# Kernel optimization log

Measured on AMD Instinct MI355X. Metric: run time of the kernel, lower is better.

The kernel has to match this reference:

```python
import jax, jax.numpy as jnp
import numpy as np


def setup_inputs() -> dict:
    key = jax.random.key(0)
    N, H, CH, T = 4, 8, 64, 2048
    qkv = jax.random.normal(key, (N, 3 * H * CH, T), dtype=jnp.float32)
    return {"qkv": qkv, "n_heads": H}


def reference(qkv, n_heads):
    bs, width, length = qkv.shape
    ch = width // (3 * n_heads)
    q, k, v = jnp.split(qkv, 3, axis=1)  # each [bs, H*ch, T]
    q = q.reshape(bs * n_heads, ch, length)
    k = k.reshape(bs * n_heads, ch, length)
    v = v.reshape(bs * n_heads, ch, length)
    scale = 1.0 / jnp.sqrt(jnp.sqrt(jnp.asarray(ch, dtype=qkv.dtype)))
    # [bs*H, T, T] score matrix (non-flash, materialized as in the original)
    weight = jnp.einsum('bct,bcs->bts', q * scale, k * scale)
    weight = jax.nn.softmax(weight.astype(jnp.float32), axis=-1).astype(qkv.dtype)
    a = jnp.einsum('bts,bcs->bct', weight, v)  # [bs*H, ch, T]
    return a.reshape(bs, n_heads * ch, length)
```

## Files before the change

### kernel.cpp

```cpp
#include <hip/hip_runtime.h>


typedef __bf16 bf8v __attribute__((ext_vector_type(8)));
typedef float f16v __attribute__((ext_vector_type(16)));
typedef int i4 __attribute__((ext_vector_type(4)));

#define SEQ 2048
#define DD 64
#define NHEADS 32
#define QBLK 128
#define SBLK 64
#define NTILES (SEQ / SBLK)
#define TILEK (SBLK * DD)
#define NTHR 256

#define KSC 0.35355339059327373f
#define QSC (0.35355339059327373f * 1.4426950408889634f)

#if __has_builtin(__builtin_amdgcn_exp2f)
#define EXP2(x) __builtin_amdgcn_exp2f(x)
#else
#define EXP2(x) exp2f(x)
#endif

__device__ __forceinline__ void gload16(i4& dst, const __bf16* p) {
    asm volatile("global_load_dwordx4 %0, %1, off" : "=&v"(dst) : "v"(p));
}

#define VMWAIT0() do { asm volatile("s_waitcnt vmcnt(0)" ::: "memory"); \
                       __builtin_amdgcn_sched_barrier(0); } while (0)
#define SBAR() __builtin_amdgcn_sched_barrier(0)

#if __has_builtin(__builtin_amdgcn_permlane32_swap)
typedef int i2v __attribute__((ext_vector_type(2)));
__device__ __forceinline__ void plswap(unsigned& a, unsigned& b) {
    i2v r = __builtin_amdgcn_permlane32_swap((int)a, (int)b, false, false);
    a = (unsigned)r.x;
    b = (unsigned)r.y;
}
#else
__device__ __forceinline__ void plswap(unsigned& a, unsigned& b) {
    asm volatile("v_permlane32_swap_b32 %0, %1" : "+v"(a), "+v"(b));
}
#endif

__global__ void prep_kernel(const float* __restrict__ qkv,
                            __bf16* __restrict__ KT, __bf16* __restrict__ Vb) {
    const int bx = blockIdx.x, tid = threadIdx.x;
    if (bx < 256) {
        const int head = bx >> 3, sblk = bx & 7;
        const int b = head >> 3, h = head & 7;
        const float* kp = qkv + (size_t)(b * 1536 + 512 + h * 64) * SEQ;
        __bf16* dst = KT + (size_t)head * SEQ * DD;
        const int s = sblk * 256 + tid;
#pragma unroll
        for (int c0 = 0; c0 < DD; c0 += 8) {
            bf8v v;
#pragma unroll
            for (int j = 0; j < 8; ++j)
                v[j] = (__bf16)(kp[(size_t)(c0 + j) * SEQ + s] * KSC);
            *(bf8v*)(dst + (size_t)s * DD + c0) = v;
        }
    } else {
        const int job = bx - 256;
        const int head = job >> 4, part = job & 15;
        const int b = head >> 3, h = head & 7;
        const float* vp = qkv + (size_t)(b * 1536 + 1024 + h * 64) * SEQ;
        __bf16* dst = Vb + (size_t)head * DD * SEQ;
#pragma unroll
        for (int i = 0; i < 4; ++i) {
            const int e = part * 8192 + (i * 256 + tid) * 8;
            const float4* f = (const float4*)(vp + e);
            float4 a = f[0], c = f[1];
            bf8v o;
            o[0] = (__bf16)a.x; o[1] = (__bf16)a.y; o[2] = (__bf16)a.z; o[3] = (__bf16)a.w;
            o[4] = (__bf16)c.x; o[5] = (__bf16)c.y; o[6] = (__bf16)c.z; o[7] = (__bf16)c.w;
            *(bf8v*)(dst + e) = o;
        }
    }
}

__device__ __forceinline__ bf8v ldswz(const __bf16* base, int r, int c16) {
    return *(const bf8v*)(base + r * DD + (((c16) ^ (r & 7)) << 3));
}

__global__ __launch_bounds__(NTHR, 2) void attn_kernel(
    const float* __restrict__ qkv, const __bf16* __restrict__ KT,
    const __bf16* __restrict__ Vb, float* __restrict__ out)
{
    __shared__ __bf16 KL[2][TILEK];
    __shared__ __bf16 VL[2][TILEK];

    const int tid = threadIdx.x;
    const int wid = tid >> 6;
    const int lane = tid & 63;
    const int hi = lane >> 5;
    const int l31 = lane & 31;

    const int bid = blockIdx.x;
    const int bx = (bid & 7) * 64 + (bid >> 3);
    const int head = bx >> 4;
    const int t0 = (bx & 15) * QBLK;
    const int b = head >> 3, h = head & 7;

    const float* qp = qkv + (size_t)(b * 1536 + h * 64) * SEQ;
    const __bf16* kt = KT + (size_t)head * SEQ * DD;
    const __bf16* vb = Vb + (size_t)head * DD * SEQ;
    float* op = out + (size_t)head * DD * SEQ;

    const int sp  = tid & 7;
    const int sr  = tid >> 3;
    const int scs = sp ^ (sr & 7);
    const __bf16* kg0 = kt + sr * DD + (scs << 3);
    const __bf16* kg1 = kt + (sr + 32) * DD + (scs << 3);
    const __bf16* vg0 = vb + (size_t)sr * SEQ + (scs << 3);
    const __bf16* vg1 = vb + (size_t)(sr + 32) * SEQ + (scs << 3);
    const int l0 = sr * DD + (sp << 3);
    const int l1 = (sr + 32) * DD + (sp << 3);

    i4 rk0, rk1, rv0, rv1;

    SBAR();
    gload16(rk0, kg0);
    gload16(rk1, kg1);
    gload16(rv0, vg0);
    gload16(rv1, vg1);
    SBAR();

    const int tq = t0 + wid * 32 + l31;
    bf8v qf[4];
#pragma unroll
    for (int kb = 0; kb < 4; ++kb) {
        bf8v q;
#pragma unroll
        for (int j = 0; j < 8; ++j)
            q[j] = (__bf16)(qp[(size_t)(kb * 16 + hi * 8 + j) * SEQ + tq] * QSC);
        qf[kb] = q;
    }

    f16v Oacc[2];
    Oacc[0] = (f16v)0.0f;
    Oacc[1] = (f16v)0.0f;
    float lp[4] = {0.f, 0.f, 0.f, 0.f};

    VMWAIT0();
    *(i4*)&KL[0][l0] = rk0;  *(i4*)&KL[0][l1] = rk1;
    *(i4*)&VL[0][l0] = rv0;  *(i4*)&VL[0][l1] = rv1;
    __syncthreads();

    for (int it = 0; it < NTILES; ++it) {
        const int cb = it & 1;
        const __bf16* kcu = KL[cb];
        const __bf16* vcu = VL[cb];
        const bool more = (it + 1 < NTILES);

        if (more) {
            const int nx = it + 1;
            SBAR();
            gload16(rk0, kg0 + nx * TILEK);
            gload16(rk1, kg1 + nx * TILEK);
            gload16(rv0, vg0 + nx * SBLK);
            gload16(rv1, vg1 + nx * SBLK);
            SBAR();
        }

        bf8v ka[2][4];
#pragma unroll
        for (int sb = 0; sb < 2; ++sb)
#pragma unroll
            for (int kb = 0; kb < 4; ++kb)
                ka[sb][kb] = ldswz(kcu, sb * 32 + l31, 2 * kb + hi);

        f16v S[2];
        S[0] = (f16v)0.0f;
        S[1] = (f16v)0.0f;
        __builtin_amdgcn_s_setprio(1);
#pragma unroll
        for (int kb = 0; kb < 4; ++kb) {
            S[0] = __builtin_amdgcn_mfma_f32_32x32x16_bf16(ka[0][kb], qf[kb], S[0], 0, 0, 0);
            S[1] = __builtin_amdgcn_mfma_f32_32x32x16_bf16(ka[1][kb], qf[kb], S[1], 0, 0, 0);
        }
        __builtin_amdgcn_s_setprio(0);

        bf8v vf[2][4];
#pragma unroll
        for (int vcb = 0; vcb < 2; ++vcb)
#pragma unroll
            for (int kb = 0; kb < 4; ++kb)
                vf[vcb][kb] = ldswz(vcu, vcb * 32 + l31, 2 * kb + hi);

        unsigned pd[2][4][2];
#pragma unroll
        for (int sb = 0; sb < 2; ++sb)
#pragma unroll
            for (int q = 0; q < 4; ++q) {
                float e0 = EXP2(S[sb][4 * q + 0]);
                float e1 = EXP2(S[sb][4 * q + 1]);
                float e2 = EXP2(S[sb][4 * q + 2]);
                float e3 = EXP2(S[sb][4 * q + 3]);
                lp[q] += (e0 + e1) + (e2 + e3);
                union { __bf16 h[2]; unsigned u; } p0, p1;
                p0.h[0] = (__bf16)e0; p0.h[1] = (__bf16)e1;
                p1.h[0] = (__bf16)e2; p1.h[1] = (__bf16)e3;
                pd[sb][q][0] = p0.u;
                pd[sb][q][1] = p1.u;
            }

#pragma unroll
        for (int sb = 0; sb < 2; ++sb)
#pragma unroll
            for (int m = 0; m < 2; ++m) {
                plswap(pd[sb][2 * m][0], pd[sb][2 * m + 1][0]);
                plswap(pd[sb][2 * m][1], pd[sb][2 * m + 1][1]);
            }

        if (more) {
            VMWAIT0();
            __bf16* kn = (__bf16*)KL[cb ^ 1];
            __bf16* vn = (__bf16*)VL[cb ^ 1];
            *(i4*)&kn[l0] = rk0;  *(i4*)&kn[l1] = rk1;
            *(i4*)&vn[l0] = rv0;  *(i4*)&vn[l1] = rv1;
            __syncthreads();
        }

        asm volatile("s_nop 2" :::);

        __builtin_amdgcn_s_setprio(1);
#pragma unroll
        for (int sb = 0; sb < 2; ++sb)
#pragma unroll
            for (int m = 0; m < 2; ++m) {
                const int kb = 2 * sb + m;
                union { unsigned u[4]; bf8v b; } f;
                f.u[0] = pd[sb][2 * m][0];
                f.u[1] = pd[sb][2 * m][1];
                f.u[2] = pd[sb][2 * m + 1][0];
                f.u[3] = pd[sb][2 * m + 1][1];
                Oacc[0] = __builtin_amdgcn_mfma_f32_32x32x16_bf16(vf[0][kb], f.b, Oacc[0], 0, 0, 0);
                Oacc[1] = __builtin_amdgcn_mfma_f32_32x32x16_bf16(vf[1][kb], f.b, Oacc[1], 0, 0, 0);
            }
        __builtin_amdgcn_s_setprio(0);
    }

    float l = (lp[0] + lp[1]) + (lp[2] + lp[3]);
    l += __shfl_xor(l, 32);
    const float rl = 1.0f / l;
#pragma unroll
    for (int cbk = 0; cbk < 2; ++cbk)
#pragma unroll
        for (int r = 0; r < 16; ++r) {
            const int row = cbk * 32 + (r & 3) + 8 * (r >> 2) + 4 * hi;
            op[(size_t)row * SEQ + tq] = Oacc[cbk][r] * rl;
        }
}

extern "C" void kernel_launch(void* const* d_in, const int* in_sizes, int n_in,
                              void* d_out, int out_size, void* d_ws, size_t ws_size,
                              hipStream_t stream) {
    const float* qkv = (const float*)d_in[0];
    float* out = (float*)d_out;
    __bf16* KT = (__bf16*)d_ws;
    __bf16* Vb = KT + (size_t)NHEADS * SEQ * DD;
    prep_kernel<<<dim3(256 + 512), dim3(NTHR), 0, stream>>>(qkv, KT, Vb);
    attn_kernel<<<dim3(NHEADS * (SEQ / QBLK)), dim3(NTHR), 0, stream>>>(qkv, KT, Vb, out);
}
```

Measured before the change: 64.76 us.

## Split key sequence across two wave groups per block and combine via LDS

Doubles the block to 512 threads and has two groups of four waves each process alternating key/value tiles for the same 128 queries. Partial outputs and row sums are merged through shared memory at the end. K/V fragment loads from LDS are moved inline next to their MFMAs to cut register pressure and allow higher occupancy. This raises the wave count per query block and the LDS use to 64KB, at the cost of an extra reduction step and more LDS traffic.

```diff
diff --git a/kernel.cpp b/kernel.cpp
--- a/kernel.cpp
+++ b/kernel.cpp
@@ -10,9 +10,9 @@
 #define NHEADS 32
 #define QBLK 128
 #define SBLK 64
-#define NTILES (SEQ / SBLK)
+#define NTILES 32
 #define TILEK (SBLK * DD)
-#define NTHR 256
+#define NTHR 512
 
 #define KSC 0.35355339059327373f
 #define QSC (0.35355339059327373f * 1.4426950408889634f)
@@ -84,15 +84,20 @@
     return *(const bf8v*)(base + r * DD + (((c16) ^ (r & 7)) << 3));
 }
 
-__global__ __launch_bounds__(NTHR, 2) void attn_kernel(
+__global__ __launch_bounds__(NTHR, 4) void attn_kernel(
     const float* __restrict__ qkv, const __bf16* __restrict__ KT,
     const __bf16* __restrict__ Vb, float* __restrict__ out)
 {
-    __shared__ __bf16 KL[2][TILEK];
-    __shared__ __bf16 VL[2][TILEK];
+    __shared__ __align__(16) char pool[65536];
+    __bf16* KLg = (__bf16*)pool;
+    __bf16* VLg = (__bf16*)(pool + 32768);
+    float* comb  = (float*)pool;
+    float* combl = (float*)(pool + 33280);
 
     const int tid = threadIdx.x;
     const int wid = tid >> 6;
+    const int gg  = wid >> 2;
+    const int qw  = wid & 3;
     const int lane = tid & 63;
     const int hi = lane >> 5;
     const int l31 = lane & 31;
@@ -108,8 +113,9 @@
     const __bf16* vb = Vb + (size_t)head * DD * SEQ;
     float* op = out + (size_t)head * DD * SEQ;
 
-    const int sp  = tid & 7;
-    const int sr  = tid >> 3;
+    const int g256 = tid & 255;
+    const int sp  = g256 & 7;
+    const int sr  = g256 >> 3;
     const int scs = sp ^ (sr & 7);
     const __bf16* kg0 = kt + sr * DD + (scs << 3);
     const __bf16* kg1 = kt + (sr + 32) * DD + (scs << 3);
@@ -121,13 +127,13 @@
     i4 rk0, rk1, rv0, rv1;
 
     SBAR();
-    gload16(rk0, kg0);
-    gload16(rk1, kg1);
-    gload16(rv0, vg0);
-    gload16(rv1, vg1);
+    gload16(rk0, kg0 + gg * TILEK);
+    gload16(rk1, kg1 + gg * TILEK);
+    gload16(rv0, vg0 + gg * SBLK);
+    gload16(rv1, vg1 + gg * SBLK);
     SBAR();
 
-    const int tq = t0 + wid * 32 + l31;
+    const int tq = t0 + qw * 32 + l31;
     bf8v qf[4];
 #pragma unroll
     for (int kb = 0; kb < 4; ++kb) {
@@ -144,60 +150,47 @@
     float lp[4] = {0.f, 0.f, 0.f, 0.f};
 
     VMWAIT0();
-    *(i4*)&KL[0][l0] = rk0;  *(i4*)&KL[0][l1] = rk1;
-    *(i4*)&VL[0][l0] = rv0;  *(i4*)&VL[0][l1] = rv1;
+    {
+        __bf16* k0 = KLg + (2 * gg) * TILEK;
+        __bf16* v0 = VLg + (2 * gg) * TILEK;
+        *(i4*)&k0[l0] = rk0;  *(i4*)&k0[l1] = rk1;
+        *(i4*)&v0[l0] = rv0;  *(i4*)&v0[l1] = rv1;
+    }
     __syncthreads();
 
-    for (int it = 0; it < NTILES; ++it) {
+    for (int it = 0; it < NTILES / 2; ++it) {
         const int cb = it & 1;
-        const __bf16* kcu = KL[cb];
-        const __bf16* vcu = VL[cb];
-        const bool more = (it + 1 < NTILES);
+        const __bf16* kcu = KLg + (2 * gg + cb) * TILEK;
+        const __bf16* vcu = VLg + (2 * gg + cb) * TILEK;
+        const bool more = (it + 1 < NTILES / 2);
 
         if (more) {
-            const int nx = it + 1;
+            const int tg = 2 * (it + 1) + gg;
             SBAR();
-            gload16(rk0, kg0 + nx * TILEK);
-            gload16(rk1, kg1 + nx * TILEK);
-            gload16(rv0, vg0 + nx * SBLK);
-            gload16(rv1, vg1 + nx * SBLK);
+            gload16(rk0, kg0 + tg * TILEK);
+            gload16(rk1, kg1 + tg * TILEK);
+            gload16(rv0, vg0 + tg * SBLK);
+            gload16(rv1, vg1 + tg * SBLK);
             SBAR();
         }
 
-        bf8v ka[2][4];
-#pragma unroll
-        for (int sb = 0; sb < 2; ++sb)
-#pragma unroll
-            for (int kb = 0; kb < 4; ++kb)
-                ka[sb][kb] = ldswz(kcu, sb * 32 + l31, 2 * kb + hi);
-
-        f16v S[2];
-        S[0] = (f16v)0.0f;
-        S[1] = (f16v)0.0f;
-        __builtin_amdgcn_s_setprio(1);
-#pragma unroll
-        for (int kb = 0; kb < 4; ++kb) {
-            S[0] = __builtin_amdgcn_mfma_f32_32x32x16_bf16(ka[0][kb], qf[kb], S[0], 0, 0, 0);
-            S[1] = __builtin_amdgcn_mfma_f32_32x32x16_bf16(ka[1][kb], qf[kb], S[1], 0, 0, 0);
-        }
-        __builtin_amdgcn_s_setprio(0);
-
-        bf8v vf[2][4];
-#pragma unroll
-        for (int vcb = 0; vcb < 2; ++vcb)
-#pragma unroll
-            for (int kb = 0; kb < 4; ++kb)
-                vf[vcb][kb] = ldswz(vcu, vcb * 32 + l31, 2 * kb + hi);
-
         unsigned pd[2][4][2];
 #pragma unroll
-        for (int sb = 0; sb < 2; ++sb)
+        for (int sb = 0; sb < 2; ++sb) {
+            f16v S = (f16v)0.0f;
+            __builtin_amdgcn_s_setprio(1);
+#pragma unroll
+            for (int kb = 0; kb < 4; ++kb) {
+                bf8v a = ldswz(kcu, sb * 32 + l31, 2 * kb + hi);
+                S = __builtin_amdgcn_mfma_f32_32x32x16_bf16(a, qf[kb], S, 0, 0, 0);
+            }
+            __builtin_amdgcn_s_setprio(0);
 #pragma unroll
             for (int q = 0; q < 4; ++q) {
-                float e0 = EXP2(S[sb][4 * q + 0]);
-                float e1 = EXP2(S[sb][4 * q + 1]);
-                float e2 = EXP2(S[sb][4 * q + 2]);
-                float e3 = EXP2(S[sb][4 * q + 3]);
+                float e0 = EXP2(S[4 * q + 0]);
+                float e1 = EXP2(S[4 * q + 1]);
+                float e2 = EXP2(S[4 * q + 2]);
+                float e3 = EXP2(S[4 * q + 3]);
                 lp[q] += (e0 + e1) + (e2 + e3);
                 union { __bf16 h[2]; unsigned u; } p0, p1;
                 p0.h[0] = (__bf16)e0; p0.h[1] = (__bf16)e1;
@@ -205,6 +198,7 @@
                 pd[sb][q][0] = p0.u;
                 pd[sb][q][1] = p1.u;
             }
+        }
 
 #pragma unroll
         for (int sb = 0; sb < 2; ++sb)
@@ -216,8 +210,8 @@
 
         if (more) {
             VMWAIT0();
-            __bf16* kn = (__bf16*)KL[cb ^ 1];
-            __bf16* vn = (__bf16*)VL[cb ^ 1];
+            __bf16* kn = KLg + (2 * gg + (cb ^ 1)) * TILEK;
+            __bf16* vn = VLg + (2 * gg + (cb ^ 1)) * TILEK;
             *(i4*)&kn[l0] = rk0;  *(i4*)&kn[l1] = rk1;
             *(i4*)&vn[l0] = rv0;  *(i4*)&vn[l1] = rv1;
             __syncthreads();
@@ -236,22 +230,41 @@
                 f.u[1] = pd[sb][2 * m][1];
                 f.u[2] = pd[sb][2 * m + 1][0];
                 f.u[3] = pd[sb][2 * m + 1][1];
-                Oacc[0] = __builtin_amdgcn_mfma_f32_32x32x16_bf16(vf[0][kb], f.b, Oacc[0], 0, 0, 0);
-                Oacc[1] = __builtin_amdgcn_mfma_f32_32x32x16_bf16(vf[1][kb], f.b, Oacc[1], 0, 0, 0);
+                bf8v v0 = ldswz(vcu, l31,      2 * kb + hi);
+                bf8v v1 = ldswz(vcu, 32 + l31, 2 * kb + hi);
+                Oacc[0] = __builtin_amdgcn_mfma_f32_32x32x16_bf16(v0, f.b, Oacc[0], 0, 0, 0);
+                Oacc[1] = __builtin_amdgcn_mfma_f32_32x32x16_bf16(v1, f.b, Oacc[1], 0, 0, 0);
             }
         __builtin_amdgcn_s_setprio(0);
     }
 
-    float l = (lp[0] + lp[1]) + (lp[2] + lp[3]);
-    l += __shfl_xor(l, 32);
-    const float rl = 1.0f / l;
-#pragma unroll
-    for (int cbk = 0; cbk < 2; ++cbk)
-#pragma unroll
-        for (int r = 0; r < 16; ++r) {
-            const int row = cbk * 32 + (r & 3) + 8 * (r >> 2) + 4 * hi;
-            op[(size_t)row * SEQ + tq] = Oacc[cbk][r] * rl;
-        }
+    float lg = (lp[0] + lp[1]) + (lp[2] + lp[3]);
+    lg += __shfl_xor(lg, 32);
+
+    __syncthreads();
+    const int qcol = qw * 32 + l31;
+    if (gg == 1) {
+#pragma unroll
+        for (int cbk = 0; cbk < 2; ++cbk)
+#pragma unroll
+            for (int r = 0; r < 16; ++r) {
+                const int c = cbk * 32 + (r & 3) + 8 * (r >> 2) + 4 * hi;
+                comb[qcol * 65 + c] = Oacc[cbk][r];
+            }
+        if (hi == 0) combl[qcol] = lg;
+    }
+    __syncthreads();
+    if (gg == 0) {
+        const float rl = 1.0f / (lg + combl[qcol]);
+#pragma unroll
+        for (int cbk = 0; cbk < 2; ++cbk)
+#pragma unroll
+            for (int r = 0; r < 16; ++r) {
+                const int c = cbk * 32 + (r & 3) + 8 * (r >> 2) + 4 * hi;
+                const float o = Oacc[cbk][r] + comb[qcol * 65 + c];
+                op[(size_t)c * SEQ + tq] = o * rl;
+            }
+    }
 }
 
 extern "C" void kernel_launch(void* const* d_in, const int* in_sizes, int n_in,
@@ -261,6 +274,6 @@
     float* out = (float*)d_out;
     __bf16* KT = (__bf16*)d_ws;
     __bf16* Vb = KT + (size_t)NHEADS * SEQ * DD;
-    prep_kernel<<<dim3(256 + 512), dim3(NTHR), 0, stream>>>(qkv, KT, Vb);
+    prep_kernel<<<dim3(256 + 512), dim3(256), 0, stream>>>(qkv, KT, Vb);
     attn_kernel<<<dim3(NHEADS * (SEQ / QBLK)), dim3(NTHR), 0, stream>>>(qkv, KT, Vb, out);
 }
```

After: 66.10 us. 2.1% more time.
